# Performance work log

Measured on AMD Instinct MI355X. Metric: run time of the kernel, lower is better.

## Reference

```python
import jax, jax.numpy as jnp
import numpy as np

B, S, K = 32, 16384, 64  # batch, num_samples, num_clusters


def _neg_idx(num_clusters):
    # Static column indices kept per row by mask_correlated_samples: drop
    # the diagonal and the (i, K+i)/(K+i, i) positive pairs -> N-2 cols/row.
    N = 2 * num_clusters
    idx = []
    for r in range(N):
        partner = r + num_clusters if r < num_clusters else r - num_clusters
        idx.append([c for c in range(N) if c != r and c != partner])
    return np.asarray(idx, dtype=np.int32)  # [N, N-2]


def target_distribution(q):
    # q: [S, K]. weight = q^2 / colsum; then row-normalize.
    w = q ** 2.0 / jnp.sum(q, axis=0)
    return w / jnp.sum(w, axis=1, keepdims=True)


def setup_inputs() -> dict:
    key = jax.random.key(0)
    k1, k2 = jax.random.split(key)
    q_i = jax.random.uniform(k1, (B, S, K), dtype=jnp.float32)
    q_j = jax.random.uniform(k2, (B, S, K), dtype=jnp.float32)
    temperature_l = jnp.asarray(1.0, dtype=jnp.float32)
    return {"q_i": q_i, "q_j": q_j, "temperature_l": temperature_l}


def reference(q_i, q_j, temperature_l):
    num_clusters = q_i.shape[2]
    N = 2 * num_clusters
    neg_idx = jnp.asarray(_neg_idx(num_clusters))  # static, [N, N-2]
    rows = jnp.arange(N)[:, None]

    def per_batch(qi_b, qj_b):
        pi = target_distribution(qi_b).T  # [K, S]
        pj = target_distribution(qj_b).T  # [K, S]
        q = jnp.concatenate([pi, pj], axis=0)        # [N, S]
        sim = jnp.matmul(q, q.T) / temperature_l      # [N, N]
        pos = jnp.concatenate(
            [jnp.diagonal(sim, num_clusters), jnp.diagonal(sim, -num_clusters)]
        )[:, None]                                    # [N, 1]
        neg = sim[rows, neg_idx]                      # [N, N-2]
        logits = jnp.concatenate([pos, neg], axis=1)  # [N, N-1], label = 0
        # CrossEntropyLoss(reduction='sum') with labels all zero
        loss = jnp.sum(jax.nn.logsumexp(logits, axis=1) - logits[:, 0])
        return loss / N

    losses = jax.vmap(per_batch)(q_i, q_j)  # [B]
    return jnp.mean(losses)
```

## Files before the change

### kernel.cpp

```cpp
#include <hip/hip_runtime.h>
#include <math.h>

#define Bn 32
#define Sn 16384
#define Kn 64
#define Nn 128

#define P1  16
#define NSB 32
#define SPB (Sn/NSB)
#define NCH (SPB/32)

typedef __attribute__((ext_vector_type(8))) short bf16x8;
typedef __attribute__((ext_vector_type(4))) float f32x4;

#define WS_CSPART 0
#define WS_GRAM   (Bn*2*P1*64)
#define WS_LOSS   (WS_GRAM + Bn*3*4096)
#define WS_PART   (WS_LOSS + Bn)
#define WS_PART_SZ ((size_t)Bn*NSB*3*4096)

__device__ __forceinline__ unsigned short f2bf(float f) {
    unsigned int u = __float_as_uint(f);
    u += 0x7FFFu + ((u >> 16) & 1u);
    return (unsigned short)(u >> 16);
}

__global__ __launch_bounds__(256) void k_colsum(const float* __restrict__ qi,
                                                const float* __restrict__ qj,
                                                float* __restrict__ ws) {
    const int blk   = blockIdx.x;
    const int chunk = blk % P1;
    const int pair  = blk / P1;
    const int v = pair & 1, b = pair >> 1;
    const float* __restrict__ src = v ? qj : qi;
    const int tid = threadIdx.x;
    const int c4 = (tid & 15) * 4;
    const int sg = tid >> 4;
    const float* __restrict__ p0 =
        src + (long)b * Sn * Kn + (long)(chunk * 16 + sg) * Kn + c4;
    const long step = (long)P1 * 16 * Kn;

    float4 acc = make_float4(0.f, 0.f, 0.f, 0.f);
    #pragma unroll 1
    for (int g = 0; g < 4; ++g) {
        float4 vv[16];
        #pragma unroll
        for (int u = 0; u < 16; ++u)
            vv[u] = *(const float4*)(p0 + (long)(g * 16 + u) * step);
        __builtin_amdgcn_sched_barrier(0);
        #pragma unroll
        for (int u = 0; u < 16; ++u) {
            acc.x += vv[u].x; acc.y += vv[u].y;
            acc.z += vv[u].z; acc.w += vv[u].w;
        }
    }
    __shared__ float red[16 * 64];
    *(float4*)&red[sg * 64 + c4] = acc;
    __syncthreads();
    if (tid < 64) {
        float s = 0.f;
        #pragma unroll
        for (int g = 0; g < 16; ++g) s += red[g * 64 + tid];
        ws[WS_CSPART + (pair * P1 + chunk) * 64 + tid] = s;
    }
}

template<int ATOMIC>
__global__ __launch_bounds__(256, 4) void k_gram(const float* __restrict__ qi,
                                                 const float* __restrict__ qj,
                                                 float* __restrict__ ws) {
    const int b   = blockIdx.x / NSB;
    const int sb  = blockIdx.x % NSB;
    const int tid = threadIdx.x;
    const int w   = tid >> 6;
    const int l   = tid & 63;
    const int lc  = tid & 15;
    const int sp  = tid >> 4;
    const int c0  = lc * 4;

    __shared__ unsigned short lp[2][2][64 * 40];
    __shared__ float csh[128];

    if (tid < 128) {
        const int view = tid >> 6, col = tid & 63;
        float s = 0.f;
        #pragma unroll
        for (int p = 0; p < P1; ++p)
            s += ws[WS_CSPART + ((b * 2 + view) * P1 + p) * 64 + col];
        csh[view * 64 + col] = s;
    }
    __syncthreads();

    const float icI[4] = {1.f / csh[c0], 1.f / csh[c0 + 1],
                          1.f / csh[c0 + 2], 1.f / csh[c0 + 3]};
    const float icJ[4] = {1.f / csh[64 + c0], 1.f / csh[64 + c0 + 1],
                          1.f / csh[64 + c0 + 2], 1.f / csh[64 + c0 + 3]};

    f32x4 aII[4], aIJ[4], aJJ[4];
    #pragma unroll
    for (int t = 0; t < 4; ++t) {
        aII[t] = (f32x4){0.f, 0.f, 0.f, 0.f};
        aIJ[t] = (f32x4){0.f, 0.f, 0.f, 0.f};
        aJJ[t] = (f32x4){0.f, 0.f, 0.f, 0.f};
    }

    const long bb  = (long)b * Sn * Kn;
    const long s0g = (long)sb * SPB;

    float4 pfa[2], pfb[2];

    auto issue = [&](int ct) {
        const long off = bb + (s0g + ct * 32 + 2 * sp) * (long)Kn + c0;
        pfa[0] = *(const float4*)(qi + off);
        pfb[0] = *(const float4*)(qi + off + Kn);
        pfa[1] = *(const float4*)(qj + off);
        pfb[1] = *(const float4*)(qj + off + Kn);
    };
    auto stage = [&](int buf) {
        #pragma unroll
        for (int v = 0; v < 2; ++v) {
            const float* ic = v ? icJ : icI;
            const float4 qa = pfa[v], qb = pfb[v];
            float wa[4] = {qa.x * qa.x * ic[0], qa.y * qa.y * ic[1],
                           qa.z * qa.z * ic[2], qa.w * qa.w * ic[3]};
            float wb[4] = {qb.x * qb.x * ic[0], qb.y * qb.y * ic[1],
                           qb.z * qb.z * ic[2], qb.w * qb.w * ic[3]};
            float ra = wa[0] + wa[1] + wa[2] + wa[3];
            float rb = wb[0] + wb[1] + wb[2] + wb[3];
            #pragma unroll
            for (int d = 1; d < 16; d <<= 1) {
                ra += __shfl_xor(ra, d);
                rb += __shfl_xor(rb, d);
            }
            const float ia = 1.f / ra, ib = 1.f / rb;
            #pragma unroll
            for (int cc = 0; cc < 4; ++cc) {
                const unsigned int pk = (unsigned int)f2bf(wa[cc] * ia)
                                      | ((unsigned int)f2bf(wb[cc] * ib) << 16);
                *(unsigned int*)&lp[buf][v][(c0 + cc) * 40 + 2 * sp] = pk;
            }
        }
    };

    issue(0);
    stage(0);
    issue(1);
    __syncthreads();

    const int sgo = (l >> 4) * 8;
    for (int ct = 0; ct < NCH; ++ct) {
        const int cur = ct & 1;
        const bf16x8 ai = *(const bf16x8*)&lp[cur][0][(w * 16 + lc) * 40 + sgo];
        const bf16x8 aj = *(const bf16x8*)&lp[cur][1][(w * 16 + lc) * 40 + sgo];
        #pragma unroll
        for (int nt = 0; nt < 4; ++nt) {
            const bf16x8 fi = *(const bf16x8*)&lp[cur][0][(nt * 16 + lc) * 40 + sgo];
            const bf16x8 fj = *(const bf16x8*)&lp[cur][1][(nt * 16 + lc) * 40 + sgo];
            aII[nt] = __builtin_amdgcn_mfma_f32_16x16x32_bf16(ai, fi, aII[nt], 0, 0, 0);
            aIJ[nt] = __builtin_amdgcn_mfma_f32_16x16x32_bf16(ai, fj, aIJ[nt], 0, 0, 0);
            aJJ[nt] = __builtin_amdgcn_mfma_f32_16x16x32_bf16(aj, fj, aJJ[nt], 0, 0, 0);
        }
        if (ct + 1 < NCH) {
            stage(cur ^ 1);
            if (ct + 2 < NCH) issue(ct + 2);
        }
        __syncthreads();
    }

    const int row0 = w * 16 + (l >> 4) * 4;
    if (ATOMIC) {
        float* __restrict__ dst = ws + WS_GRAM + (long)b * 3 * 4096;
        #pragma unroll
        for (int nt = 0; nt < 4; ++nt) {
            #pragma unroll
            for (int r = 0; r < 4; ++r) {
                const int e = (row0 + r) * 64 + nt * 16 + lc;
                atomicAdd(&dst[e],        aII[nt][r]);
                atomicAdd(&dst[4096 + e], aIJ[nt][r]);
                atomicAdd(&dst[8192 + e], aJJ[nt][r]);
            }
        }
    } else {
        float* __restrict__ dst = ws + WS_PART + (long)(b * NSB + sb) * 3 * 4096;
        #pragma unroll
        for (int nt = 0; nt < 4; ++nt) {
            #pragma unroll
            for (int r = 0; r < 4; ++r) {
                const int e = (row0 + r) * 64 + nt * 16 + lc;
                dst[e]        = aII[nt][r];
                dst[4096 + e] = aIJ[nt][r];
                dst[8192 + e] = aJJ[nt][r];
            }
        }
    }
}

__global__ __launch_bounds__(256) void k_gram_reduce(float* __restrict__ ws) {
    const int idx = blockIdx.x * 256 + threadIdx.x;
    const int b = idx / (3 * 4096);
    const int e = idx % (3 * 4096);
    float s = 0.f;
    #pragma unroll 8
    for (int p = 0; p < NSB; ++p)
        s += ws[WS_PART + (long)(b * NSB + p) * 3 * 4096 + e];
    ws[WS_GRAM + (long)b * 3 * 4096 + e] = s;
}

__device__ __forceinline__ float sim_entry(const float* __restrict__ g, int r, int c) {
    if (r < 64) return (c < 64) ? g[r * 64 + c] : g[4096 + r * 64 + (c - 64)];
    return (c < 64) ? g[4096 + c * 64 + (r - 64)] : g[8192 + (r - 64) * 64 + (c - 64)];
}

__global__ __launch_bounds__(128) void k_loss(const float* __restrict__ temp,
                                              float* __restrict__ ws) {
    const int b = blockIdx.x;
    const int r = threadIdx.x;
    const float* __restrict__ g = ws + WS_GRAM + (long)b * 3 * 4096;
    const float inv_t = 1.f / temp[0];
    const int p = r ^ 64;

    float m = -1e30f, pos = 0.f;
    for (int c = 0; c < Nn; ++c) {
        if (c == r) continue;
        const float v = sim_entry(g, r, c) * inv_t;
        m = fmaxf(m, v);
        if (c == p) pos = v;
    }
    float sum = 0.f;
    for (int c = 0; c < Nn; ++c) {
        if (c == r) continue;
        const float v = sim_entry(g, r, c) * inv_t;
        sum += expf(v - m);
    }
    const float val = m + logf(sum) - pos;

    __shared__ float red[Nn];
    red[r] = val;
    __syncthreads();
    for (int st = 64; st > 0; st >>= 1) {
        if (r < st) red[r] += red[r + st];
        __syncthreads();
    }
    if (r == 0) ws[WS_LOSS + b] = red[0] / (float)Nn;
}

__global__ void k_final(float* __restrict__ ws, float* __restrict__ out) {
    if (threadIdx.x == 0) {
        float s = 0.f;
        for (int b = 0; b < Bn; ++b) s += ws[WS_LOSS + b];
        out[0] = s / (float)Bn;
    }
}

extern "C" void kernel_launch(void* const* d_in, const int* in_sizes, int n_in,
                              void* d_out, int out_size, void* d_ws, size_t ws_size,
                              hipStream_t stream) {
    const float* qi   = (const float*)d_in[0];
    const float* qj   = (const float*)d_in[1];
    const float* temp = (const float*)d_in[2];
    float* ws  = (float*)d_ws;
    float* out = (float*)d_out;

    const size_t need_f = (size_t)WS_PART + WS_PART_SZ;
    const bool partial = ws_size >= need_f * sizeof(float);

    k_colsum<<<Bn * 2 * P1, 256, 0, stream>>>(qi, qj, ws);

    if (partial) {
        k_gram<0><<<Bn * NSB, 256, 0, stream>>>(qi, qj, ws);
        k_gram_reduce<<<(Bn * 3 * 4096) / 256, 256, 0, stream>>>(ws);
    } else {
        hipMemsetAsync(ws + WS_GRAM, 0, (size_t)Bn * 3 * 4096 * sizeof(float), stream);
        k_gram<1><<<Bn * NSB, 256, 0, stream>>>(qi, qj, ws);
    }

    k_loss<<<Bn, 128, 0, stream>>>(temp, ws);
    k_final<<<1, 64, 0, stream>>>(ws, out);
}
```

Baseline: 166.6 us.

## Stream colsum input through LDS with async global_load_lds double buffering

Rewrites the column-sum kernel so each wave streams contiguous row blocks into LDS with global_load_lds and a two-buffer vmcnt-gated pipeline, instead of strided float4 register loads. It also halves the number of chunks per batch/view, giving each block twice as many rows. The goal is contiguous, deeper in-flight memory traffic for the bandwidth-bound colsum pass. It also adds unroll 1 on the gram main loop. The costs are fewer blocks, which lowers parallelism, and reliance on hand-written waitcnt ordering.

```diff
diff --git a/kernel.cpp b/kernel.cpp
--- a/kernel.cpp
+++ b/kernel.cpp
@@ -6,7 +6,7 @@
 #define Kn 64
 #define Nn 128
 
-#define P1  16
+#define P1  8
 #define NSB 32
 #define SPB (Sn/NSB)
 #define NCH (SPB/32)
@@ -24,6 +24,12 @@
     unsigned int u = __float_as_uint(f);
     u += 0x7FFFu + ((u >> 16) & 1u);
     return (unsigned short)(u >> 16);
+}
+
+__device__ __forceinline__ void glds16(const float* gp, float* lp) {
+    __builtin_amdgcn_global_load_lds(
+        (const __attribute__((address_space(1))) void*)gp,
+        (__attribute__((address_space(3))) void*)lp, 16, 0, 0);
 }
 
 __global__ __launch_bounds__(256) void k_colsum(const float* __restrict__ qi,
@@ -35,33 +41,46 @@
     const int v = pair & 1, b = pair >> 1;
     const float* __restrict__ src = v ? qj : qi;
     const int tid = threadIdx.x;
-    const int c4 = (tid & 15) * 4;
-    const int sg = tid >> 4;
-    const float* __restrict__ p0 =
-        src + (long)b * Sn * Kn + (long)(chunk * 16 + sg) * Kn + c4;
-    const long step = (long)P1 * 16 * Kn;
-
-    float4 acc = make_float4(0.f, 0.f, 0.f, 0.f);
+    const int w = tid >> 6, l = tid & 63;
+
+    __shared__ float stg[4][2][2048];
+    __shared__ float red[4][4][64];
+
+    const float* __restrict__ gbase =
+        src + (long)b * Sn * Kn + (long)(chunk * (Sn / P1)) * Kn + l * 4;
+
+    auto issueHalf = [&](int h, int buf) {
+        const float* gp = gbase + (long)(w * 512 + h * 32) * Kn;
+        float* lp = &stg[w][buf][0];
+        #pragma unroll
+        for (int k = 0; k < 8; ++k)
+            glds16(gp + (long)k * 4 * Kn, lp + k * 256);
+    };
+
+    f32x4 acc = {0.f, 0.f, 0.f, 0.f};
+
+    issueHalf(0, 0);
+    issueHalf(1, 1);
     #pragma unroll 1
-    for (int g = 0; g < 4; ++g) {
-        float4 vv[16];
-        #pragma unroll
-        for (int u = 0; u < 16; ++u)
-            vv[u] = *(const float4*)(p0 + (long)(g * 16 + u) * step);
+    for (int h = 0; h < 16; ++h) {
+        const int buf = h & 1;
+        if (h + 1 < 16) asm volatile("s_waitcnt vmcnt(8)" ::: "memory");
+        else            asm volatile("s_waitcnt vmcnt(0)" ::: "memory");
         __builtin_amdgcn_sched_barrier(0);
         #pragma unroll
-        for (int u = 0; u < 16; ++u) {
-            acc.x += vv[u].x; acc.y += vv[u].y;
-            acc.z += vv[u].z; acc.w += vv[u].w;
-        }
-    }
-    __shared__ float red[16 * 64];
-    *(float4*)&red[sg * 64 + c4] = acc;
+        for (int k = 0; k < 8; ++k)
+            acc += *(const f32x4*)&stg[w][buf][k * 256 + l * 4];
+        asm volatile("s_waitcnt lgkmcnt(0)" ::: "memory");
+        __builtin_amdgcn_sched_barrier(0);
+        if (h + 2 < 16) issueHalf(h + 2, buf);
+    }
+
+    *(f32x4*)&red[w][l >> 4][(l & 15) * 4] = acc;
     __syncthreads();
     if (tid < 64) {
         float s = 0.f;
         #pragma unroll
-        for (int g = 0; g < 16; ++g) s += red[g * 64 + tid];
+        for (int g = 0; g < 16; ++g) s += red[g >> 2][g & 3][tid];
         ws[WS_CSPART + (pair * P1 + chunk) * 64 + tid] = s;
     }
 }
@@ -149,6 +168,7 @@
     __syncthreads();
 
     const int sgo = (l >> 4) * 8;
+    #pragma unroll 1
     for (int ct = 0; ct < NCH; ++ct) {
         const int cur = ct & 1;
         const bf16x8 ai = *(const bf16x8*)&lp[cur][0][(w * 16 + lc) * 40 + sgo];
```

Measured after the change: 169.7 us. No clear change (+1.9%).
